# Kernel optimization log

Hardware: AMD Instinct MI355X
Metric: run time of the kernel (lower is better)

Reference implementation:

```python
import jax, jax.numpy as jnp
import numpy as np

K, T, RHO, V, TH, EH, S, B = 50, 50, 300, 20000, 800, 200, 10, 256
DELTA = 0.005
LOG_DELTA = float(np.log(DELTA))
EPS = 1e-6


def setup_inputs() -> dict:
    key = jax.random.key(0)
    ks = jax.random.split(key, 32)
    f32 = jnp.float32
    rn = lambda i, shp, s=0.02: jax.random.normal(ks[i], shp, f32) * s
    inp = {
        "unique_tokens": jax.random.randint(ks[0], (100,), 0, V),
        "bows": jax.random.uniform(ks[1], (B, V), f32),
        "normalized_bows": jax.random.uniform(ks[2], (B, V), f32),
        "times": jax.random.randint(ks[3], (B,), 0, T),
        "sources": jax.random.randint(ks[4], (B,), 0, S),
        "rnn_inp": jax.random.normal(ks[5], (S, T, V), f32),
        "num_docs": 100000,
        # learned parameters
        "mu_q_alpha": rn(6, (K, T, RHO), 1.0),
        "logsigma_q_alpha": rn(7, (K, T, RHO), 0.1),
        "rho_W": rn(8, (V, RHO)),                 # Linear(rho_size -> vocab, no bias)
        "W1": rn(9, (TH, V + K)), "b1": jnp.zeros((TH,), f32),
        "W2": rn(10, (TH, TH)), "b2": jnp.zeros((TH,), f32),
        "mu_th_W": rn(11, (K, TH)), "mu_th_b": jnp.zeros((K,), f32),
        "ls_th_W": rn(12, (K, TH)), "ls_th_b": jnp.zeros((K,), f32),
        "eta_map_W": rn(13, (EH, V)), "eta_map_b": jnp.zeros((EH,), f32),
        "lstm_Wih": rn(14, (4 * EH, EH)), "lstm_Whh": rn(15, (4 * EH, EH)),
        "lstm_bih": jnp.zeros((4 * EH,), f32), "lstm_bhh": jnp.zeros((4 * EH,), f32),
        "mu_eta_W": rn(16, (K, EH + K)), "mu_eta_b": jnp.zeros((K,), f32),
        "ls_eta_W": rn(17, (K, EH + K)), "ls_eta_b": jnp.zeros((K,), f32),
        "cls_W": rn(18, (S, K)), "cls_b": jnp.zeros((S,), f32),
    }
    return inp


def _lstm(x_seq, Wih, Whh, bih, bhh):
    # x_seq: [T, S, EH]; torch gate order i,f,g,o
    def step(carry, x):
        h, c = carry
        z = x @ Wih.T + bih + h @ Whh.T + bhh
        i, f, g, o = jnp.split(z, 4, axis=-1)
        c = jax.nn.sigmoid(f) * c + jax.nn.sigmoid(i) * jnp.tanh(g)
        h = jax.nn.sigmoid(o) * jnp.tanh(c)
        return (h, c), h
    h0 = jnp.zeros((x_seq.shape[1], Whh.shape[1]), x_seq.dtype)
    _, out = jax.lax.scan(step, (h0, h0), x_seq)
    return out  # [T, S, EH]


def reference(unique_tokens, bows, normalized_bows, times, sources, rnn_inp, num_docs,
              mu_q_alpha, logsigma_q_alpha, rho_W, W1, b1, W2, b2,
              mu_th_W, mu_th_b, ls_th_W, ls_th_b, eta_map_W, eta_map_b,
              lstm_Wih, lstm_Whh, lstm_bih, lstm_bhh,
              mu_eta_W, mu_eta_b, ls_eta_W, ls_eta_b, cls_W, cls_b):
    # eval-mode semantics: reparameterize returns mu, dropout off
    bsz = bows.shape[0]
    coeff = num_docs / bsz

    # ---- alpha: eval-mode alphas_t == mu_q_alpha[:, t, :]; KL vectorized ----
    mu_a, ls_a = mu_q_alpha, logsigma_q_alpha  # [K, T, RHO]
    kl_a0 = 0.5 * jnp.sum((jnp.exp(ls_a[:, 0]) + mu_a[:, 0] ** 2) / (1.0 + EPS) - 1.0 - ls_a[:, 0])
    diff = mu_a[:, 1:] - mu_a[:, :-1]
    kl_at = 0.5 * jnp.sum((jnp.exp(ls_a[:, 1:]) + diff ** 2) / (DELTA + EPS) - 1.0 + LOG_DELTA - ls_a[:, 1:])
    kl_alpha = kl_a0 + kl_at
    alphas = jnp.transpose(mu_a, (1, 0, 2))  # [T, K, RHO]

    # ---- eta: LSTM over time (vmapped over sources as batch), then recurrence ----
    mapped = jnp.einsum('stv,hv->sth', rnn_inp, eta_map_W) + eta_map_b  # [S, T, EH]
    lstm_out = _lstm(jnp.transpose(mapped, (1, 0, 2)), lstm_Wih, lstm_Whh, lstm_bih, lstm_bhh)  # [T, S, EH]

    inp0 = jnp.concatenate([lstm_out[0], jnp.zeros((S, K), lstm_out.dtype)], axis=-1)
    mu0 = inp0 @ mu_eta_W.T + mu_eta_b
    ls0 = inp0 @ ls_eta_W.T + ls_eta_b  # no clipping at t=0 in original
    kl0 = 0.5 * jnp.sum((jnp.exp(ls0) + mu0 ** 2) / (1.0 + EPS) - 1.0 - ls0)

    def eta_step(carry, out_t):
        eta_prev, kl = carry
        inp_t = jnp.concatenate([out_t, eta_prev], axis=-1)
        mu_t = inp_t @ mu_eta_W.T + mu_eta_b
        ls_t = jnp.clip(inp_t @ ls_eta_W.T + ls_eta_b, -10.0, 10.0)
        kl_t = 0.5 * jnp.sum((jnp.exp(ls_t) + (mu_t - eta_prev) ** 2) / (DELTA + EPS) - 1.0 + LOG_DELTA - ls_t)
        return (mu_t, kl + kl_t), mu_t
    (_, kl_rest), etas_rest = jax.lax.scan(eta_step, (mu0, jnp.float32(0.0)), lstm_out[1:])
    etas = jnp.transpose(jnp.concatenate([mu0[None], etas_rest], axis=0), (1, 0, 2))  # [S, T, K]
    kl_eta = kl0 + kl_rest

    # ---- theta ----
    eta_std = etas[sources, times]  # [B, K]
    h = jax.nn.relu(jnp.concatenate([normalized_bows, eta_std], axis=1) @ W1.T + b1)
    h = jax.nn.relu(h @ W2.T + b2)
    mu_t = h @ mu_th_W.T + mu_th_b
    ls_t = jnp.clip(h @ ls_th_W.T + ls_th_b, -10.0, 10.0)
    theta = jax.nn.softmax(mu_t, axis=-1)
    kl_theta = (0.5 * jnp.sum((jnp.exp(ls_t) + (mu_t - eta_std) ** 2) / (1.0 + EPS) - 1.0 - ls_t)) * coeff

    # ---- beta and NLL ----
    logit = jnp.einsum('tkr,vr->tkv', alphas, rho_W)
    beta = jax.nn.softmax(logit, axis=-1)        # [T, K, V]
    beta_d = beta[times]                         # [B, K, V]
    loglik = jnp.log(jnp.einsum('bk,bkv->bv', theta, beta_d))
    nll = -jnp.sum(loglik * bows) * coeff

    # ---- source prediction loss (sum-reduced cross entropy) ----
    logits = theta @ cls_W.T + cls_b
    logp = jax.nn.log_softmax(logits, axis=-1)
    pred_loss = -jnp.sum(jnp.take_along_axis(logp, sources[:, None], axis=1)) * coeff

    nelbo = nll + kl_alpha + kl_eta + kl_theta + pred_loss
    return (nelbo, nll, kl_alpha, kl_eta, kl_theta, pred_loss)
```

## Files before the change

### kernel.cpp

```cpp
#include <hip/hip_runtime.h>

typedef unsigned int u32;
typedef unsigned short ushort_t;

#define NTOP 50
#define NT_T 50
#define NRHO 300
#define NVOC 20000
#define NTH 800
#define NEH 200
#define NSRC 10
#define NBAT 256

#define OFF_SCAL     0
#define OFF_MAPPED   16
#define OFF_HPRE     100016
#define OFF_H2       304816
#define OFF_Z        509616
#define OFF_DOCCNT   512120
#define OFF_DOCLIST  512176
#define MEMSET_BYTES ((size_t)524976 * 4)
#define OFF_XW       524976
#define OFF_BIAS2    924976
#define OFF_ETAS     925776
#define OFF_WCOEF    950776
#define OFF_W1E      963576
#define OFF_WHH_H    1003576
#define OFF_ETAWH    1083576
#define OFF_H1B      1096376
#define OFF_MAPB     1198776
#define OFF_WIHB     1256120
#define OFF_W2B      1356472
#define OFF_ALPHAB   1714872
#define OFF_RHOB     2124472
#define OFF_NBB      5339832
#define OFF_W1B      7899832
#define OFF_RNNB     16859832
#define OFF_EMWB     21979832
#define OFF_LOGITH   7899832

typedef _Float16 h2v __attribute__((ext_vector_type(2)));
typedef __bf16 bf16x8 __attribute__((ext_vector_type(8)));
typedef float f32x4 __attribute__((ext_vector_type(4)));

#define REP25(M) M(0) M(1) M(2) M(3) M(4) M(5) M(6) M(7) M(8) M(9) M(10) M(11) M(12) \
                 M(13) M(14) M(15) M(16) M(17) M(18) M(19) M(20) M(21) M(22) M(23) M(24)
#define REP7(M) M(0) M(1) M(2) M(3) M(4) M(5) M(6)

__device__ inline float dot2u(u32 a, u32 b, float c){
  h2v ha = __builtin_bit_cast(h2v, a), hb = __builtin_bit_cast(h2v, b);
#if __has_builtin(__builtin_amdgcn_fdot2)
  return __builtin_amdgcn_fdot2(ha, hb, c, false);
#else
  return c + (float)ha.x*(float)hb.x + (float)ha.y*(float)hb.y;
#endif
}

__device__ inline u32 packh2(float lo, float hi){
  h2v h; h.x = (_Float16)lo; h.y = (_Float16)hi;
  return __builtin_bit_cast(u32, h);
}

__device__ inline ushort_t f2bf(float f){
  u32 u = __builtin_bit_cast(u32, f);
  u = (u + 0x7FFFu + ((u >> 16) & 1u)) >> 16;
  return (ushort_t)u;
}

__device__ inline float fast_sig(float x){ return 1.f/(1.f + __expf(-x)); }
__device__ inline float fast_tanh(float x){ float e = __expf(2.f*x); return 1.f - 2.f/(e + 1.f); }

__device__ __forceinline__ void gl2lds16(const void* g, void* l){
  __builtin_amdgcn_global_load_lds((__attribute__((address_space(1))) void*)g,
                                   (__attribute__((address_space(3))) void*)l,
                                   16, 0, 0);
}

__device__ inline void blockReduceAdd(float v, float* red, float* target){
  int tid = threadIdx.x;
  red[tid] = v; __syncthreads();
  for (int o = blockDim.x >> 1; o > 0; o >>= 1){
    if (tid < o) red[tid] += red[tid + o];
    __syncthreads();
  }
  if (tid == 0) atomicAdd(target, red[0]);
}

__device__ inline void conv_seg(const float* __restrict__ src, int ldsrc,
                                int Mreal, int Kused,
                                ushort_t* __restrict__ dst, int Kp, int idx)
{
  int kb = Kp >> 3;
  int row = idx / kb, c = (idx - row*kb) << 3;
  ushort_t out[8];
  #pragma unroll
  for (int j = 0; j < 8; j++){
    float v = 0.f;
    int k = c + j;
    if (row < Mreal && k < Kused) v = src[(size_t)row*ldsrc + k];
    out[j] = f2bf(v);
  }
  *(uint4*)(dst + (size_t)row*Kp + c) = *(uint4*)out;
}

__global__ __launch_bounds__(256) void k_mega(
    const float* __restrict__ whh,
    const float* __restrict__ muEW, const float* __restrict__ lsEW,
    const float* __restrict__ bih, const float* __restrict__ bhh,
    const float* __restrict__ wih, const float* __restrict__ emapB,
    const float* __restrict__ W1, const int* __restrict__ times,
    const float* __restrict__ muq, const float* __restrict__ lsq,
    const float* __restrict__ rho, const float* __restrict__ nb,
    const float* __restrict__ rnn, const float* __restrict__ emapW,
    const float* __restrict__ W2f, float* __restrict__ W)
{
  int b = blockIdx.x, tid = threadIdx.x;
  __shared__ float red[256];
  if (b < 523){
    int idx = b*256 + tid;
    u32* whhH = (u32*)(W + OFF_WHH_H);
    u32* etaWH = (u32*)(W + OFF_ETAWH);
    if (idx < 80000){
      int j = idx/100; int i = idx - j*100;
      whhH[idx] = packh2(whh[j*200 + 2*i], whh[j*200 + 2*i + 1]);
    } else if (idx < 92800){
      int d = idx - 80000; int q = d >> 7; int i = d & 127;
      u32 v = 0u;
      if (i < 125){
        const float* src = (q < 50) ? (muEW + q*250) : (lsEW + (q-50)*250);
        v = packh2(src[2*i], src[2*i+1]);
      }
      etaWH[d] = v;
    } else if (idx < 93600){
      int j = idx - 92800;
      float acc = bih[j] + bhh[j];
      const float* wr = wih + (size_t)j*200;
      #pragma unroll 4
      for (int k = 0; k < 200; k++) acc += emapB[k]*wr[k];
      W[OFF_BIAS2 + j] = acc;
    } else if (idx < 133600){
      int d = idx - 93600; int j = d/50; int k = d - j*50;
      W[OFF_W1E + d] = W1[(size_t)j*20050 + 20000 + k];
    } else if (idx < 133856){
      int bb = idx - 133600; int t = times[bb];
      int* docCnt = (int*)(W + OFF_DOCCNT);
      int* docList = (int*)(W + OFF_DOCLIST);
      int pos = atomicAdd(&docCnt[t], 1);
      docList[t*256 + pos] = bb;
    }
  } else if (b < 923){
    int idx = (b-523)*256 + tid;
    int row = idx / 40, c = (idx - row*40) << 3;
    ushort_t out[8];
    const float* src = nullptr;
    if (row < 2500){ int t = row/50, k = row - t*50; src = muq + (size_t)k*15000 + t*300; }
    #pragma unroll
    for (int j = 0; j < 8; j++){
      int r = c + j;
      float v = (src && r < 300) ? src[r] : 0.f;
      out[j] = f2bf(v);
    }
    *(uint4*)((ushort_t*)(W + OFF_ALPHAB) + (size_t)row*320 + c) = *(uint4*)out;
  } else if (b < 4063){
    conv_seg(rho, 300, 20000, 300, (ushort_t*)(W + OFF_RHOB), 320, (b-923)*256 + tid);
  } else if (b < 6563){
    conv_seg(nb, 20000, 256, 20000, (ushort_t*)(W + OFF_NBB), 20000, (b-4063)*256 + tid);
  } else if (b < 15313){
    conv_seg(W1, 20050, 800, 20000, (ushort_t*)(W + OFF_W1B), 20000, (b-6563)*256 + tid);
  } else if (b < 20313){
    conv_seg(rnn, 20000, 500, 20000, (ushort_t*)(W + OFF_RNNB), 20000, (b-15313)*256 + tid);
  } else if (b < 22813){
    conv_seg(emapW, 20000, 200, 20000, (ushort_t*)(W + OFF_EMWB), 20000, (b-20313)*256 + tid);
  } else if (b < 22911){
    conv_seg(wih, 200, 800, 200, (ushort_t*)(W + OFF_WIHB), 224, (b-22813)*256 + tid);
  } else if (b < 23261){
    conv_seg(W2f, 800, 800, 800, (ushort_t*)(W + OFF_W2B), 800, (b-22911)*256 + tid);
  } else {
    const float inv_dl = 1.f/(0.005f + 1e-6f);
    const float logdl = -5.2983173665480363f;
    float local = 0.f;
    for (int idx = (b-23261)*256 + tid; idx < 750000; idx += 1024*256){
      int rem = idx % 15000; int t = rem / 300;
      float ls = lsq[idx]; float mu = muq[idx];
      if (t == 0){
        local += 0.5f*((__expf(ls) + mu*mu)/(1.f + 1e-6f) - 1.f - ls);
      } else {
        float d = mu - muq[idx - 300];
        local += 0.5f*((__expf(ls) + d*d)*inv_dl - 1.f + logdl - ls);
      }
    }
    blockReduceAdd(local, red, W + OFF_SCAL + 1);
  }
}

__global__ __launch_bounds__(256) void k_conv(const float* __restrict__ src, int ldsrc,
                                              int Mreal, int Kused,
                                              ushort_t* __restrict__ dst, int Mp, int Kp)
{
  int idx = blockIdx.x*256 + threadIdx.x;
  int kb = Kp >> 3;
  if (idx >= Mp*kb) return;
  conv_seg(src, ldsrc, Mreal, Kused, dst, Kp, idx);
}

template<int MODE>
__global__ __launch_bounds__(256) void mfma_nt(
    const ushort_t* __restrict__ A, int lda,
    const ushort_t* __restrict__ B, int ldb,
    float* __restrict__ C, _Float16* __restrict__ Ch, int ldc,
    const float* __restrict__ nBias,
    int M, int N, int mT, int kS, int chunks)
{
  __shared__ __align__(16) ushort_t As[128*32];
  __shared__ __align__(16) ushort_t Bs[128*32];
  int bid = blockIdx.x;
  int kIdx = bid % kS; int rest = bid / kS;
  int mIdx = rest % mT; int nIdx = rest / mT;
  int tid = threadIdx.x;
  int w = tid >> 6, l = tid & 63;
  int c0 = (int)(((long long)chunks * kIdx) / kS);
  int c1 = (int)(((long long)chunks * (kIdx+1)) / kS);
  int r0 = w*32;
  const ushort_t* ga0 = A + (size_t)(mIdx*128 + r0      + (l>>2))*lda + (l&3)*8;
  const ushort_t* ga1 = A + (size_t)(mIdx*128 + r0 + 16 + (l>>2))*lda + (l&3)*8;
  const ushort_t* gb0 = B + (size_t)(nIdx*128 + r0      + (l>>2))*ldb + (l&3)*8;
  const ushort_t* gb1 = B + (size_t)(nIdx*128 + r0 + 16 + (l>>2))*ldb + (l&3)*8;
  ushort_t* la = As + r0*32;
  ushort_t* lb = Bs + r0*32;
  int wr = (w >> 1)*64, wc = (w & 1)*64;
  int lr = l & 15, lq = l >> 4;
  f32x4 acc[4][4];
  #pragma unroll
  for (int i = 0; i < 4; i++)
    #pragma unroll
    for (int j = 0; j < 4; j++)
      acc[i][j] = (f32x4)0.f;

  for (int c = c0; c < c1; c++){
    size_t ko = (size_t)c * 32;
    gl2lds16(ga0 + ko, la);
    gl2lds16(ga1 + ko, la + 512);
    gl2lds16(gb0 + ko, lb);
    gl2lds16(gb1 + ko, lb + 512);
    __syncthreads();
    bf16x8 av[4], bv[4];
    #pragma unroll
    for (int i = 0; i < 4; i++)
      av[i] = *(const bf16x8*)(As + (wr + i*16 + lr)*32 + lq*8);
    #pragma unroll
    for (int j = 0; j < 4; j++)
      bv[j] = *(const bf16x8*)(Bs + (wc + j*16 + lr)*32 + lq*8);
    #pragma unroll
    for (int i = 0; i < 4; i++)
      #pragma unroll
      for (int j = 0; j < 4; j++)
        acc[i][j] = __builtin_amdgcn_mfma_f32_16x16x32_bf16(av[i], bv[j], acc[i][j], 0, 0, 0);
    __syncthreads();
  }
  if (MODE == 3){
    float* Z = C;
    #pragma unroll
    for (int i = 0; i < 4; i++){
      #pragma unroll
      for (int r = 0; r < 4; r++){
        int row = mIdx*128 + wr + i*16 + lq*4 + r;
        float p = 0.f;
        if (row < M){
          #pragma unroll
          for (int j = 0; j < 4; j++){
            int col = nIdx*128 + wc + j*16 + lr;
            if (col < N){
              float e = __expf(acc[i][j][r]);
              Ch[(size_t)row*ldc + col] = (_Float16)e;
              p += e;
            }
          }
        }
        p += __shfl_xor(p, 1, 16);
        p += __shfl_xor(p, 2, 16);
        p += __shfl_xor(p, 4, 16);
        p += __shfl_xor(p, 8, 16);
        if (lr == 0 && row < M) atomicAdd(&Z[row], p);
      }
    }
  } else {
    #pragma unroll
    for (int i = 0; i < 4; i++){
      #pragma unroll
      for (int r = 0; r < 4; r++){
        int row = mIdx*128 + wr + i*16 + lq*4 + r;
        if (row >= M) continue;
        #pragma unroll
        for (int j = 0; j < 4; j++){
          int col = nIdx*128 + wc + j*16 + lr;
          if (col >= N) continue;
          float v = acc[i][j][r];
          if (MODE == 0)      atomicAdd(&C[(size_t)row*ldc + col], v);
          else                C[(size_t)row*ldc + col] = v + nBias[col];
        }
      }
    }
  }
}

__global__ __launch_bounds__(512, 2) void k_lstm(
    const float* __restrict__ xw, const u32* __restrict__ whhH, const uint4* __restrict__ etaW4,
    const float* __restrict__ muEB, const float* __restrict__ lsEB,
    float* __restrict__ etas, float* __restrict__ W)
{
  int s = blockIdx.x; int tid = threadIdx.x;
  __shared__ uint4 hp4[2][32];
  __shared__ float zbuf[800];
  __shared__ float red[512];
  uint4 z4; z4.x = z4.y = z4.z = z4.w = 0u;
#define DECLW(i) uint4 wa##i = z4, wb##i = z4;
  REP25(DECLW)
#undef DECLW
  float ebias = 0.f;
  if (tid < 400){
    const uint4* ra = (const uint4*)(whhH + tid*100);
    const uint4* rb = (const uint4*)(whhH + (tid + 400)*100);
#define LDW(i) wa##i = ra[i]; wb##i = rb[i];
    REP25(LDW)
#undef LDW
  } else if (tid < 500){
    int q = tid - 400;
    const uint4* re = etaW4 + q*32;
#define LDA(i) wa##i = re[i];
    REP25(LDA)
#undef LDA
#define LDB(i) wb##i = re[25+i];
    REP7(LDB)
#undef LDB
    ebias = (q < 50) ? muEB[q] : lsEB[q - 50];
  }
  float creg = 0.f, muPrev = 0.f, klLocal = 0.f;
  if (tid < 64) ((uint4*)hp4)[tid] = z4;
  __syncthreads();
  const float inv_dl = 1.f/(0.005f + 1e-6f);
  const float logdl = -5.2983173665480363f;

  for (int t = 0; t < NT_T; t++){
    const uint4* hc = hp4[t & 1];
    uint4* hn = hp4[(t + 1) & 1];
    if (tid < 400){
      float a0=0.f,a1=0.f,a2=0.f,a3=0.f,b0=0.f,b1=0.f,b2=0.f,b3=0.f;
#define DOT(i) { uint4 h = hc[i]; \
      a0 = dot2u(wa##i.x, h.x, a0); a1 = dot2u(wa##i.y, h.y, a1); \
      a2 = dot2u(wa##i.z, h.z, a2); a3 = dot2u(wa##i.w, h.w, a3); \
      b0 = dot2u(wb##i.x, h.x, b0); b1 = dot2u(wb##i.y, h.y, b1); \
      b2 = dot2u(wb##i.z, h.z, b2); b3 = dot2u(wb##i.w, h.w, b3); }
      REP25(DOT)
#undef DOT
      const float* xr = xw + (size_t)(s*50 + t)*800;
      zbuf[tid]       = ((a0+a1)+(a2+a3)) + xr[tid];
      zbuf[tid + 400] = ((b0+b1)+(b2+b3)) + xr[tid + 400];
    }
    __syncthreads();
    if (tid < 200){
      float zi = zbuf[tid], zf = zbuf[200+tid], zg = zbuf[400+tid], zo = zbuf[600+tid];
      float ig = fast_sig(zi);
      float fg = fast_sig(zf);
      float gg = fast_tanh(zg);
      float og = fast_sig(zo);
      creg = fg*creg + ig*gg;
      float hv = og*fast_tanh(creg);
      ((_Float16*)hn)[tid] = (_Float16)hv;
    }
    __syncthreads();
    if (tid >= 400 && tid < 500){
      float e0 = ebias, e1 = 0.f, e2 = 0.f, e3 = 0.f;
#define DOTE(i) { uint4 h = hn[i]; \
      e0 = dot2u(wa##i.x, h.x, e0); e1 = dot2u(wa##i.y, h.y, e1); \
      e2 = dot2u(wa##i.z, h.z, e2); e3 = dot2u(wa##i.w, h.w, e3); }
      REP25(DOTE)
#undef DOTE
#define DOTP(i) { uint4 h = hc[25+i]; \
      e0 = dot2u(wb##i.x, h.x, e0); e1 = dot2u(wb##i.y, h.y, e1); \
      e2 = dot2u(wb##i.z, h.z, e2); e3 = dot2u(wb##i.w, h.w, e3); }
      REP7(DOTP)
#undef DOTP
      float eacc = (e0+e1)+(e2+e3);
      int q = tid - 400;
      if (q < 50){
        float mu = eacc;
        etas[(size_t)(s*50 + t)*50 + q] = mu;
        if (t == 0) klLocal += 0.5f*mu*mu/(1.f + 1e-6f);
        else { float d = mu - muPrev; klLocal += 0.5f*d*d*inv_dl; }
        muPrev = mu;
        ((_Float16*)hn)[200 + q] = (_Float16)mu;
      } else {
        float ls = eacc;
        if (t == 0) klLocal += 0.5f*(__expf(ls)/(1.f + 1e-6f) - 1.f - ls);
        else {
          ls = fminf(fmaxf(ls, -10.f), 10.f);
          klLocal += 0.5f*(__expf(ls)*inv_dl - 1.f + logdl - ls);
        }
      }
    }
  }
  __syncthreads();
  blockReduceAdd(klLocal, red, W + OFF_SCAL + 2);
}

__global__ __launch_bounds__(256) void k_h1(
    const float* __restrict__ hpre, const float* __restrict__ b1, const float* __restrict__ w1e,
    const float* __restrict__ etas, const int* __restrict__ times, const int* __restrict__ srcs,
    ushort_t* __restrict__ h1B)
{
  int b = blockIdx.x, tid = threadIdx.x;
  __shared__ float et[50];
  int tb = times[b], sb = srcs[b];
  if (tid < 50) et[tid] = etas[(size_t)(sb*50 + tb)*50 + tid];
  __syncthreads();
  for (int j = tid; j < 800; j += 256){
    float acc = hpre[(size_t)b*800 + j] + b1[j];
    const float* wrow = w1e + (size_t)j*50;
    #pragma unroll
    for (int k = 0; k < 50; k++) acc += et[k]*wrow[k];
    h1B[(size_t)b*800 + j] = f2bf(fmaxf(acc, 0.f));
  }
}

__global__ __launch_bounds__(256) void k_thfin(
    const float* __restrict__ h2g, const float* __restrict__ b2, const float* __restrict__ etas,
    const int* __restrict__ times, const int* __restrict__ srcs,
    const float* __restrict__ muW, const float* __restrict__ muB,
    const float* __restrict__ lsW, const float* __restrict__ lsB,
    const float* __restrict__ clsW, const float* __restrict__ clsB,
    const float* __restrict__ Zrow, float* __restrict__ wcoef, float* __restrict__ W)
{
  int b = blockIdx.x, tid = threadIdx.x;
  __shared__ float h2s[800], mu[50], lsv[50], et[50], th[50], lg[10], red[64], shm[2];
  for (int j = tid; j < 800; j += 256) h2s[j] = fmaxf(h2g[(size_t)b*800 + j] + b2[j], 0.f);
  int tb = times[b], sb = srcs[b];
  if (tid < 50) et[tid] = etas[(size_t)(sb*50 + tb)*50 + tid];
  __syncthreads();
  if (tid < 100){
    int q = (tid < 50) ? tid : tid - 50;
    const float* w = (tid < 50) ? (muW + (size_t)q*800) : (lsW + (size_t)q*800);
    float acc = (tid < 50) ? muB[q] : lsB[q];
    #pragma unroll 8
    for (int j = 0; j < 800; j++) acc += h2s[j]*w[j];
    if (tid < 50) mu[q] = acc;
    else lsv[q] = fminf(fmaxf(acc, -10.f), 10.f);
  }
  __syncthreads();
  if (tid == 0){ float m = -1e30f; for (int k = 0; k < 50; k++) m = fmaxf(m, mu[k]); shm[0] = m; }
  __syncthreads();
  if (tid < 50) th[tid] = __expf(mu[tid] - shm[0]);
  __syncthreads();
  if (tid == 0){ float z = 0.f; for (int k = 0; k < 50; k++) z += th[k]; shm[1] = z; }
  __syncthreads();
  if (tid < 64) red[tid] = 0.f;
  if (tid < 50){
    float t_ = th[tid]/shm[1]; th[tid] = t_;
    wcoef[(size_t)b*50 + tid] = t_/Zrow[tb*50 + tid];
    float d = mu[tid] - et[tid];
    red[tid] = 0.5f*((__expf(lsv[tid]) + d*d)/(1.f + 1e-6f) - 1.f - lsv[tid]);
  }
  __syncthreads();
  if (tid < 10){
    float a = clsB[tid];
    #pragma unroll
    for (int k = 0; k < 50; k++) a += th[k]*clsW[tid*50 + k];
    lg[tid] = a;
  }
  __syncthreads();
  if (tid == 0){
    float m = -1e30f; for (int i = 0; i < 10; i++) m = fmaxf(m, lg[i]);
    float z = 0.f; for (int i = 0; i < 10; i++) z += __expf(lg[i] - m);
    float lse = m + __logf(z);
    atomicAdd(W + OFF_SCAL + 4, lse - lg[sb]);
    float ssum = 0.f; for (int i = 0; i < 50; i++) ssum += red[i];
    atomicAdd(W + OFF_SCAL + 3, ssum);
  }
}

__global__ __launch_bounds__(256) void k_nll(
    const _Float16* __restrict__ E, const float* __restrict__ wcoef,
    const float* __restrict__ bows, float* __restrict__ W)
{
  int t = blockIdx.x/10, vc = blockIdx.x%10;
  int v0 = vc*2000;
  int tid = threadIdx.x;
  const int* docCnt = (const int*)(W + OFF_DOCCNT);
  const int* docList = (const int*)(W + OFF_DOCLIST);
  __shared__ float wch[64*50];
  __shared__ int ids[64];
  __shared__ float red[256];
  int nd = docCnt[t];
  float acc = 0.f;
  for (int d0 = 0; d0 < nd; d0 += 64){
    int ndc = min(64, nd - d0);
    __syncthreads();
    for (int i = tid; i < ndc*50; i += 256){
      int d = i/50, k = i - d*50;
      int bb = docList[t*256 + d0 + d];
      if (k == 0) ids[d] = bb;
      wch[i] = wcoef[(size_t)bb*50 + k];
    }
    __syncthreads();
    for (int v = v0 + tid; v < v0 + 2000; v += 256){
      float e[50];
      #pragma unroll
      for (int k = 0; k < 50; k++)
        e[k] = (float)E[(size_t)(t*50 + k)*NVOC + v];
      for (int d = 0; d < ndc; d++){
        float s = 0.f;
        #pragma unroll
        for (int k = 0; k < 50; k++) s += wch[d*50 + k]*e[k];
        acc += bows[(size_t)ids[d]*NVOC + v]*__logf(s);
      }
    }
  }
  __syncthreads();
  blockReduceAdd(acc, red, W + OFF_SCAL + 0);
}

__global__ void k_final(const float* __restrict__ W, const int* __restrict__ ndocs, float* __restrict__ out)
{
  if (blockIdx.x == 0 && threadIdx.x == 0){
    float coeff = (float)ndocs[0] / 256.f;
    const float* scal = W + OFF_SCAL;
    float nll  = -scal[0]*coeff;
    float kla  = scal[1];
    float kle  = scal[2];
    float klth = scal[3]*coeff;
    float pred = scal[4]*coeff;
    out[0] = nll + kla + kle + klth + pred;
    out[1] = nll; out[2] = kla; out[3] = kle; out[4] = klth; out[5] = pred;
  }
}

extern "C" void kernel_launch(void* const* d_in, const int* in_sizes, int n_in,
                              void* d_out, int out_size, void* d_ws, size_t ws_size,
                              hipStream_t stream)
{
  (void)in_sizes; (void)n_in; (void)out_size; (void)ws_size;
  const float* bows  = (const float*)d_in[1];
  const float* nb    = (const float*)d_in[2];
  const int*   times = (const int*)d_in[3];
  const int*   srcs  = (const int*)d_in[4];
  const float* rnn   = (const float*)d_in[5];
  const int*   ndocs = (const int*)d_in[6];
  const float* muq   = (const float*)d_in[7];
  const float* lsq   = (const float*)d_in[8];
  const float* rho   = (const float*)d_in[9];
  const float* W1    = (const float*)d_in[10];
  const float* b1    = (const float*)d_in[11];
  const float* W2    = (const float*)d_in[12];
  const float* b2    = (const float*)d_in[13];
  const float* muthW = (const float*)d_in[14];
  const float* muthB = (const float*)d_in[15];
  const float* lsthW = (const float*)d_in[16];
  const float* lsthB = (const float*)d_in[17];
  const float* emapW = (const float*)d_in[18];
  const float* emapB = (const float*)d_in[19];
  const float* wih   = (const float*)d_in[20];
  const float* whh   = (const float*)d_in[21];
  const float* bih   = (const float*)d_in[22];
  const float* bhh   = (const float*)d_in[23];
  const float* muEW  = (const float*)d_in[24];
  const float* muEB  = (const float*)d_in[25];
  const float* lsEW  = (const float*)d_in[26];
  const float* lsEB  = (const float*)d_in[27];
  const float* clsW  = (const float*)d_in[28];
  const float* clsB  = (const float*)d_in[29];

  float* W = (float*)d_ws;
  ushort_t* alphaB = (ushort_t*)(W + OFF_ALPHAB);
  ushort_t* rhoB   = (ushort_t*)(W + OFF_RHOB);
  ushort_t* nbB    = (ushort_t*)(W + OFF_NBB);
  ushort_t* w1B    = (ushort_t*)(W + OFF_W1B);
  ushort_t* rnnB   = (ushort_t*)(W + OFF_RNNB);
  ushort_t* emwB   = (ushort_t*)(W + OFF_EMWB);
  ushort_t* wihB   = (ushort_t*)(W + OFF_WIHB);
  ushort_t* w2B    = (ushort_t*)(W + OFF_W2B);
  ushort_t* mapB   = (ushort_t*)(W + OFF_MAPB);
  ushort_t* h1B    = (ushort_t*)(W + OFF_H1B);
  _Float16* Ehalf  = (_Float16*)(W + OFF_LOGITH);

  hipMemsetAsync(d_ws, 0, MEMSET_BYTES, stream);

  k_mega<<<24285, 256, 0, stream>>>(whh, muEW, lsEW, bih, bhh, wih, emapB, W1, times,
                                    muq, lsq, rho, nb, rnn, emapW, W2, W);

  mfma_nt<0><<<4*2*32, 256, 0, stream>>>(
      rnnB, 20000, emwB, 20000, W + OFF_MAPPED, nullptr, 200, nullptr,
      500, 200, 4, 32, 625);

  mfma_nt<0><<<2*7*20, 256, 0, stream>>>(
      nbB, 20000, w1B, 20000, W + OFF_HPRE, nullptr, 800, nullptr,
      256, 800, 2, 20, 625);

  mfma_nt<3><<<20*157, 256, 0, stream>>>(
      alphaB, 320, rhoB, 320, W + OFF_Z, Ehalf, 20000, nullptr,
      2500, 20000, 20, 1, 10);

  k_conv<<<56, 256, 0, stream>>>(W + OFF_MAPPED, 200, 500, 200, mapB, 512, 224);

  mfma_nt<2><<<4*7, 256, 0, stream>>>(
      mapB, 224, wihB, 224, W + OFF_XW, nullptr, 800, W + OFF_BIAS2,
      500, 800, 4, 1, 7);

  k_lstm<<<NSRC, 512, 0, stream>>>(W + OFF_XW, (const u32*)(W + OFF_WHH_H),
                                   (const uint4*)(W + OFF_ETAWH), muEB, lsEB,
                                   W + OFF_ETAS, W);

  k_h1<<<256, 256, 0, stream>>>(W + OFF_HPRE, b1, W + OFF_W1E, W + OFF_ETAS, times, srcs, h1B);

  mfma_nt<0><<<2*7*2, 256, 0, stream>>>(
      h1B, 800, w2B, 800, W + OFF_H2, nullptr, 800, nullptr,
      256, 800, 2, 2, 25);

  k_thfin<<<256, 256, 0, stream>>>(W + OFF_H2, b2, W + OFF_ETAS, times, srcs,
                                   muthW, muthB, lsthW, lsthB, clsW, clsB,
                                   W + OFF_Z, W + OFF_WCOEF, W);

  k_nll<<<500, 256, 0, stream>>>(Ehalf, W + OFF_WCOEF, bows, W);

  k_final<<<1, 64, 0, stream>>>(W, ndocs, (float*)d_out);
}
```

Before: 710.2 us.

## Double-buffer LDS tiles in MFMA GEMM to overlap global loads with compute

```diff
diff --git a/kernel.cpp b/kernel.cpp
--- a/kernel.cpp
+++ b/kernel.cpp
@@ -211,8 +211,8 @@
     const float* __restrict__ nBias,
     int M, int N, int mT, int kS, int chunks)
 {
-  __shared__ __align__(16) ushort_t As[128*32];
-  __shared__ __align__(16) ushort_t Bs[128*32];
+  __shared__ __align__(16) ushort_t As[2][128*32];
+  __shared__ __align__(16) ushort_t Bs[2][128*32];
   int bid = blockIdx.x;
   int kIdx = bid % kS; int rest = bid / kS;
   int mIdx = rest % mT; int nIdx = rest / mT;
@@ -225,8 +225,6 @@
   const ushort_t* ga1 = A + (size_t)(mIdx*128 + r0 + 16 + (l>>2))*lda + (l&3)*8;
   const ushort_t* gb0 = B + (size_t)(nIdx*128 + r0      + (l>>2))*ldb + (l&3)*8;
   const ushort_t* gb1 = B + (size_t)(nIdx*128 + r0 + 16 + (l>>2))*ldb + (l&3)*8;
-  ushort_t* la = As + r0*32;
-  ushort_t* lb = Bs + r0*32;
   int wr = (w >> 1)*64, wc = (w & 1)*64;
   int lr = l & 15, lq = l >> 4;
   f32x4 acc[4][4];
@@ -236,26 +234,41 @@
     for (int j = 0; j < 4; j++)
       acc[i][j] = (f32x4)0.f;
 
+  {
+    size_t ko = (size_t)c0 * 32;
+    gl2lds16(ga0 + ko, As[0] + r0*32);
+    gl2lds16(ga1 + ko, As[0] + r0*32 + 512);
+    gl2lds16(gb0 + ko, Bs[0] + r0*32);
+    gl2lds16(gb1 + ko, Bs[0] + r0*32 + 512);
+  }
+  asm volatile("s_waitcnt vmcnt(0)" ::: "memory");
+  __builtin_amdgcn_s_barrier();
+
+  int cur = 0;
   for (int c = c0; c < c1; c++){
-    size_t ko = (size_t)c * 32;
-    gl2lds16(ga0 + ko, la);
-    gl2lds16(ga1 + ko, la + 512);
-    gl2lds16(gb0 + ko, lb);
-    gl2lds16(gb1 + ko, lb + 512);
-    __syncthreads();
+    if (c + 1 < c1){
+      size_t ko = (size_t)(c + 1) * 32;
+      int nxt = cur ^ 1;
+      gl2lds16(ga0 + ko, As[nxt] + r0*32);
+      gl2lds16(ga1 + ko, As[nxt] + r0*32 + 512);
+      gl2lds16(gb0 + ko, Bs[nxt] + r0*32);
+      gl2lds16(gb1 + ko, Bs[nxt] + r0*32 + 512);
+    }
     bf16x8 av[4], bv[4];
     #pragma unroll
     for (int i = 0; i < 4; i++)
-      av[i] = *(const bf16x8*)(As + (wr + i*16 + lr)*32 + lq*8);
+      av[i] = *(const bf16x8*)(As[cur] + (wr + i*16 + lr)*32 + lq*8);
     #pragma unroll
     for (int j = 0; j < 4; j++)
-      bv[j] = *(const bf16x8*)(Bs + (wc + j*16 + lr)*32 + lq*8);
+      bv[j] = *(const bf16x8*)(Bs[cur] + (wc + j*16 + lr)*32 + lq*8);
     #pragma unroll
     for (int i = 0; i < 4; i++)
       #pragma unroll
       for (int j = 0; j < 4; j++)
         acc[i][j] = __builtin_amdgcn_mfma_f32_16x16x32_bf16(av[i], bv[j], acc[i][j], 0, 0, 0);
-    __syncthreads();
+    asm volatile("s_waitcnt vmcnt(0)" ::: "memory");
+    __builtin_amdgcn_s_barrier();
+    cur ^= 1;
   }
   if (MODE == 3){
     float* Z = C;
```

New measurement: 708.7 us. No clear change (-0.2%).
